# Kernel optimization log

Hardware: AMD Instinct MI355X
Metric: run time of the kernel (lower is better)

## Reference

```python
import jax, jax.numpy as jnp
import numpy as np

H, N, B, L = 256, 64, 4, 2048
LN_EPS = 1e-5


def setup_inputs() -> dict:
    key = jax.random.key(0)
    ks = jax.random.split(key, 10)
    u = jax.random.normal(ks[0], (B, L, H), dtype=jnp.float32)
    # Parameters (HiPPO-eig init replaced by equivalent-range random init; same forward math).
    log_neg_real = jnp.log(jax.random.uniform(ks[1], (N,), minval=0.01, maxval=2.0))
    imag = jax.random.normal(ks[2], (N,)) * 3.0
    B_re = jax.random.normal(ks[3], (H, N)) * 0.01
    B_im = jax.random.normal(ks[4], (H, N)) * 0.01
    C_re = jax.random.normal(ks[5], (H, N)) * 0.01
    C_im = jax.random.normal(ks[6], (H, N)) * 0.01
    D = jax.random.normal(ks[7], (H,)) * 0.01
    log_step = jax.random.uniform(ks[8], (H,), minval=-4.0, maxval=-1.0)
    ln_gamma = jnp.ones((H,), dtype=jnp.float32)
    ln_beta = jnp.zeros((H,), dtype=jnp.float32)
    return {"u": u, "log_neg_real": log_neg_real, "imag": imag,
            "B_re": B_re, "B_im": B_im, "C_re": C_re, "C_im": C_im,
            "D": D, "log_step": log_step, "ln_gamma": ln_gamma, "ln_beta": ln_beta}


def reference(u, log_neg_real, imag, B_re, B_im, C_re, C_im, D, log_step, ln_gamma, ln_beta):
    Bb, Ll, Hh = u.shape
    Lam_re = -jnp.exp(log_neg_real)                      # (N,)
    step = jnp.clip(jnp.exp(log_step), 1e-5, 1.0)        # (H,)
    s_re = step[:, None] * Lam_re[None, :]               # (H,N)
    s_im = step[:, None] * imag[None, :]                 # (H,N)
    Bb_re = B_re * step[:, None]
    Bb_im = B_im * step[:, None]
    CB_re = C_re * Bb_re - C_im * Bb_im                  # (H,N)
    CB_im = C_re * Bb_im + C_im * Bb_re                  # (H,N)
    l_idx = jnp.arange(Ll, dtype=u.dtype)                # (L,)
    ls_re = s_re[:, None, :] * l_idx[None, :, None]      # (H,L,N)
    ls_im = s_im[:, None, :] * l_idx[None, :, None]      # (H,L,N)
    mag = jnp.exp(ls_re)
    K = (jnp.einsum('hn,hln->hl', CB_re, mag * jnp.cos(ls_im))
         - jnp.einsum('hn,hln->hl', CB_im, mag * jnp.sin(ls_im)))  # (H,L)
    # FFT circular conv with zero padding to 2L -> linear conv
    uT = jnp.transpose(u, (0, 2, 1))                     # (B,H,L)
    n = 2 * Ll
    u_f = jnp.fft.rfft(uT, n=n)
    K_f = jnp.fft.rfft(K, n=n)
    y = jnp.fft.irfft(u_f * K_f[None], n=n)[..., :Ll]    # (B,H,L)
    y = y + uT * D[None, :, None]
    y = jnp.transpose(y, (0, 2, 1))                      # (B,L,H)
    y = jax.nn.gelu(y, approximate=False)                # torch nn.GELU default = exact
    # dropout: eval mode (identity)
    mean = jnp.mean(y, axis=-1, keepdims=True)
    var = jnp.var(y, axis=-1, keepdims=True)
    y = (y - mean) / jnp.sqrt(var + LN_EPS) * ln_gamma + ln_beta
    return y
```

## Files before the change

kernel.cpp:

```cpp
#include <hip/hip_runtime.h>
#include <hip/hip_bf16.h>
#include <math.h>

#define Hn 256
#define Nn 64
#define Bn 4
#define Ln 2048
#define Cn 64
#define NC 32

__global__ __launch_bounds__(256)
void k_pre(const float* __restrict__ u, float* __restrict__ uT,
           const float* __restrict__ lnr, const float* __restrict__ im,
           const float* __restrict__ Bre, const float* __restrict__ Bim,
           const float* __restrict__ Cre, const float* __restrict__ Cim,
           const float* __restrict__ lstep,
           float* __restrict__ G, float* __restrict__ apar,
           float* __restrict__ Krow)
{
    __shared__ float sh[64 * 65];
    int bid = blockIdx.x;
    int t   = threadIdx.x;

    if (bid < 512) {
        int b  = bid >> 7;
        int h0 = ((bid >> 5) & 3) << 6;
        int l0 = (bid & 31) << 6;
        int c4 = t & 15, rr = t >> 4;
        #pragma unroll
        for (int i = 0; i < 4; ++i) {
            int r = rr + (i << 4);
            float4 v = *(const float4*)&u[((size_t)b * Ln + l0 + r) * Hn + h0 + (c4 << 2)];
            sh[r * 65 + (c4 << 2) + 0] = v.x;
            sh[r * 65 + (c4 << 2) + 1] = v.y;
            sh[r * 65 + (c4 << 2) + 2] = v.z;
            sh[r * 65 + (c4 << 2) + 3] = v.w;
        }
        __syncthreads();
        #pragma unroll
        for (int i = 0; i < 4; ++i) {
            int hr = (t >> 4) + (i << 4);
            int lc = t & 15;
            float4 v;
            v.x = sh[((lc << 2) + 0) * 65 + hr];
            v.y = sh[((lc << 2) + 1) * 65 + hr];
            v.z = sh[((lc << 2) + 2) * 65 + hr];
            v.w = sh[((lc << 2) + 3) * 65 + hr];
            *(float4*)&uT[((size_t)b * Hn + h0 + hr) * Ln + l0 + (lc << 2)] = v;
        }
    } else {
        int h = bid - 512;
        int n = t;
        if (t < 64) {
            float st  = fminf(fmaxf(expf(lstep[h]), 1e-5f), 1.0f);
            float lam = -expf(lnr[n]);
            float er  = expf(st * lam);
            float sim = st * im[n];
            float ar  = er * cosf(sim);
            float ai  = er * sinf(sim);
            float bre = Bre[h * Nn + n] * st;
            float bim = Bim[h * Nn + n] * st;
            float cr  = Cre[h * Nn + n];
            float ci  = Cim[h * Nn + n];
            float CBr = cr * bre - ci * bim;
            float CBi = cr * bim + ci * bre;

            *(float2*)&apar[(h * Nn + n) * 2] = make_float2(ar, ai);

            float Pr = ar, Pi = ai;
            float Qr = 1.f, Qi = 0.f;
            for (int j = 0; j < 64; ++j) {
                *(float2*)&G[((h * 64 + j) * 64 + n) * 2] =
                    make_float2(CBr * Pr - CBi * Pi, CBr * Pi + CBi * Pr);
                sh[j * 65 + n] = CBr * Qr - CBi * Qi;
                float npr = Pr * ar - Pi * ai; Pi = Pr * ai + Pi * ar; Pr = npr;
                float nqr = Qr * ar - Qi * ai; Qi = Qr * ai + Qi * ar; Qr = nqr;
            }
        }
        __syncthreads();
        if (t < 64) {
            float s = 0.f;
            #pragma unroll
            for (int m = 0; m < 64; ++m) s += sh[t * 65 + m];
            Krow[h * 64 + t] = s;
        }
    }
}

__global__ __launch_bounds__(256, 4)
void k_scan_chunks(const float* __restrict__ uT, const float* __restrict__ apar,
                   const float* __restrict__ G, const float* __restrict__ Krow,
                   const float* __restrict__ D, float* __restrict__ ypre)
{
    int bh  = blockIdx.x;
    int h   = bh & (Hn - 1);
    int tid = threadIdx.x;
    int j   = tid & 63;
    int w   = __builtin_amdgcn_readfirstlane(tid >> 6);
    int n0  = w << 4;

    __shared__ float  kbuf[128];
    __shared__ float2 S_lds[NC][64];
    __shared__ float2 F_lds[4][64];
    __shared__ float  part[16][4][64];

    if (tid < 64) kbuf[tid] = 0.f;
    else if (tid < 128) kbuf[tid] = Krow[h * 64 + tid - 64];

    int n = j;
    float ar = apar[(h * Nn + n) * 2];
    float ai = apar[(h * Nn + n) * 2 + 1];
    float a2r = ar * ar - ai * ai;
    float a2i = 2.f * ar * ai;
    const float* uRow = uT + (size_t)bh * Ln;
    const float* useg = uRow + (w << 9);

    float2 Sloc[8];
    float xr = 0.f, xi = 0.f;
    #pragma unroll
    for (int k = 0; k < 8; ++k) {
        Sloc[k] = make_float2(xr, xi);
        const float4* up4 = (const float4*)(useg + (k << 6));
        #pragma unroll
        for (int q = 0; q < 16; ++q) {
            float4 uu = up4[q];
            float crr = fmaf(ar, uu.x, uu.y);
            float cii = ai * uu.x;
            float nxr = fmaf(a2r, xr, fmaf(-a2i, xi, crr));
            float nxi = fmaf(a2i, xr, fmaf(a2r, xi, cii));
            xr = nxr; xi = nxi;
            crr = fmaf(ar, uu.z, uu.w);
            cii = ai * uu.z;
            nxr = fmaf(a2r, xr, fmaf(-a2i, xi, crr));
            nxi = fmaf(a2i, xr, fmaf(a2r, xi, cii));
            xr = nxr; xi = nxi;
        }
    }
    F_lds[w][n] = make_float2(xr, xi);
    __syncthreads();

    float b_r = ar, b_i = ai;
    #pragma unroll
    for (int q = 0; q < 6; ++q) { float nr = b_r * b_r - b_i * b_i; b_i = 2.f * b_r * b_i; b_r = nr; }
    float p_r = b_r, p_i = b_i;
    #pragma unroll
    for (int q = 0; q < 3; ++q) { float nr = p_r * p_r - p_i * p_i; p_i = 2.f * p_r * p_i; p_r = nr; }

    float Xr = 0.f, Xi = 0.f;
    for (int s = 0; s < w; ++s) {
        float2 Ft = F_lds[s][n];
        float nXr = fmaf(p_r, Xr, fmaf(-p_i, Xi, Ft.x));
        float nXi = fmaf(p_i, Xr, fmaf(p_r, Xi, Ft.y));
        Xr = nXr; Xi = nXi;
    }

    float e_r = 1.f, e_i = 0.f;
    #pragma unroll
    for (int k = 0; k < 8; ++k) {
        float sr = Sloc[k].x + (e_r * Xr - e_i * Xi);
        float si = Sloc[k].y + (e_r * Xi + e_i * Xr);
        S_lds[(w << 3) + k][n] = make_float2(sr, si);
        float nr = e_r * b_r - e_i * b_i;
        e_i = e_r * b_i + e_i * b_r;
        e_r = nr;
    }
    __syncthreads();

    float4 Gr4[8];
    const float4* Gp4 = (const float4*)((const float2*)G + ((h * 64 + j) * 64 + n0));
    #pragma unroll
    for (int i = 0; i < 8; ++i) Gr4[i] = Gp4[i];
    float Kreg[16];
    #pragma unroll
    for (int i = 0; i < 16; ++i) Kreg[i] = kbuf[64 + j - n0 - i];

    float Dh = D[h];

    for (int half = 0; half < 2; ++half) {
        for (int cc = 0; cc < 16; ++cc) {
            int c = (half << 4) | cc;
            const float4* Sp4 = (const float4*)&S_lds[c][n0];
            const float4* uc4 = (const float4*)(uRow + (c << 6) + n0);
            float y0 = 0.f, y1 = 0.f, y2 = 0.f;
            #pragma unroll
            for (int i = 0; i < 8; ++i) {
                float4 sv = Sp4[i];
                y0 = fmaf(Gr4[i].x, sv.x, y0);
                y1 = fmaf(-Gr4[i].y, sv.y, y1);
                y0 = fmaf(Gr4[i].z, sv.z, y0);
                y1 = fmaf(-Gr4[i].w, sv.w, y1);
            }
            #pragma unroll
            for (int i = 0; i < 4; ++i) {
                float4 uu = uc4[i];
                y2 = fmaf(Kreg[4 * i + 0], uu.x, y2);
                y2 = fmaf(Kreg[4 * i + 1], uu.y, y2);
                y2 = fmaf(Kreg[4 * i + 2], uu.z, y2);
                y2 = fmaf(Kreg[4 * i + 3], uu.w, y2);
            }
            part[cc][w][j] = (y0 + y1) + y2;
        }
        __syncthreads();
        #pragma unroll
        for (int k = 0; k < 4; ++k) {
            int cc = (k << 2) | w;
            int c  = (half << 4) | cc;
            float y  = (part[cc][0][j] + part[cc][1][j]) + (part[cc][2][j] + part[cc][3][j]);
            float uv = uRow[(c << 6) + j];
            float yv = fmaf(Dh, uv, y);
            float g  = 0.5f * yv * (1.f + erff(yv * 0.70710678118654752f));
            ypre[(size_t)bh * Ln + (c << 6) + j] = g;
        }
        __syncthreads();
    }
}

__global__ __launch_bounds__(256)
void k_ln(const float* __restrict__ ypre, const float* __restrict__ gamma,
          const float* __restrict__ beta, float* __restrict__ out)
{
    __shared__ float tile[32][260];
    int b  = blockIdx.y;
    int l0 = blockIdx.x << 5;
    int t  = threadIdx.x;

    #pragma unroll
    for (int i = 0; i < 8; ++i) {
        int idx = (i << 8) + t;
        int hh  = idx >> 3, lo4 = idx & 7;
        float4 v = *(const float4*)&ypre[((size_t)b * Hn + hh) * Ln + l0 + (lo4 << 2)];
        tile[(lo4 << 2) + 0][hh] = v.x;
        tile[(lo4 << 2) + 1][hh] = v.y;
        tile[(lo4 << 2) + 2][hh] = v.z;
        tile[(lo4 << 2) + 3][hh] = v.w;
    }
    __syncthreads();

    int wv = t >> 6, lane = t & 63;
    float4 g4 = *(const float4*)&gamma[lane << 2];
    float4 b4 = *(const float4*)&beta[lane << 2];
    #pragma unroll
    for (int k = 0; k < 8; ++k) {
        int l = (k << 2) | wv;
        float4 v = *(const float4*)&tile[l][lane << 2];
        float sum = (v.x + v.y) + (v.z + v.w);
        float sq  = fmaf(v.x, v.x, fmaf(v.y, v.y, fmaf(v.z, v.z, v.w * v.w)));
        #pragma unroll
        for (int off = 32; off; off >>= 1) {
            sum += __shfl_xor(sum, off);
            sq  += __shfl_xor(sq, off);
        }
        float mean = sum * (1.f / 256.f);
        float var  = sq * (1.f / 256.f) - mean * mean;
        float rs   = rsqrtf(var + 1e-5f);
        float4 o;
        o.x = (v.x - mean) * rs * g4.x + b4.x;
        o.y = (v.y - mean) * rs * g4.y + b4.y;
        o.z = (v.z - mean) * rs * g4.z + b4.z;
        o.w = (v.w - mean) * rs * g4.w + b4.w;
        *(float4*)&out[((size_t)b * Ln + l0 + l) * Hn + (lane << 2)] = o;
    }
}

extern "C" void kernel_launch(void* const* d_in, const int* in_sizes, int n_in,
                              void* d_out, int out_size, void* d_ws, size_t ws_size,
                              hipStream_t stream)
{
    const float* u     = (const float*)d_in[0];
    const float* lnr   = (const float*)d_in[1];
    const float* im    = (const float*)d_in[2];
    const float* Bre   = (const float*)d_in[3];
    const float* Bim   = (const float*)d_in[4];
    const float* Cre   = (const float*)d_in[5];
    const float* Cim   = (const float*)d_in[6];
    const float* Dp    = (const float*)d_in[7];
    const float* lstep = (const float*)d_in[8];
    const float* gam   = (const float*)d_in[9];
    const float* bet   = (const float*)d_in[10];
    float* out = (float*)d_out;

    float* ws   = (float*)d_ws;
    float* uT   = ws;
    float* G    = uT   + (size_t)Bn * Hn * Ln;
    float* apar = G    + (size_t)Hn * 64 * Nn * 2;
    float* Krow = apar + (size_t)Hn * Nn * 2;
    float* ypre = Krow + (size_t)Hn * 64;

    k_pre<<<768, 256, 0, stream>>>(u, uT, lnr, im, Bre, Bim, Cre, Cim, lstep, G, apar, Krow);
    k_scan_chunks<<<Bn * Hn, 256, 0, stream>>>(uT, apar, G, Krow, Dp, ypre);
    k_ln<<<dim3(Ln / 32, Bn), 256, 0, stream>>>(ypre, gam, bet, out);
}
```

Before: 123.6 us.

## Recast chunked SSM scan as split-bf16 MFMA matmuls with precomputed fragments

```diff
diff --git a/kernel.cpp b/kernel.cpp
--- a/kernel.cpp
+++ b/kernel.cpp
@@ -6,8 +6,28 @@
 #define Nn 64
 #define Bn 4
 #define Ln 2048
-#define Cn 64
 #define NC 32
+
+typedef __attribute__((ext_vector_type(8))) short short8;
+typedef __attribute__((ext_vector_type(4))) float f32x4;
+
+#define MFMA16 __builtin_amdgcn_mfma_f32_16x16x32_bf16
+
+#define AF1_STRIDE 16384
+#define AF2_STRIDE 24576
+
+__device__ inline short bf16hi(float x) {
+    union { __hip_bfloat16 b; unsigned short u; } cv;
+    cv.b = __float2bfloat16(x);
+    return (short)cv.u;
+}
+__device__ inline float bf16f(short s) {
+    union { __hip_bfloat16 b; unsigned short u; } cv;
+    cv.u = (unsigned short)s;
+    return __bfloat162float(cv.b);
+}
+
+#define CSQ(r, i) { float _nr = (r)*(r) - (i)*(i); (i) = 2.f*(r)*(i); (r) = _nr; }
 
 __global__ __launch_bounds__(256)
 void k_pre(const float* __restrict__ u, float* __restrict__ uT,
@@ -15,203 +35,279 @@
            const float* __restrict__ Bre, const float* __restrict__ Bim,
            const float* __restrict__ Cre, const float* __restrict__ Cim,
            const float* __restrict__ lstep,
-           float* __restrict__ G, float* __restrict__ apar,
-           float* __restrict__ Krow)
+           short* __restrict__ AF1, short* __restrict__ AF2,
+           float* __restrict__ apar)
 {
-    __shared__ float sh[64 * 65];
+    __shared__ float sh[2][64][66];
+    __shared__ float cbrL[64];
+    __shared__ float kb[128];
     int bid = blockIdx.x;
-    int t   = threadIdx.x;
+    int tid = threadIdx.x;
 
     if (bid < 512) {
         int b  = bid >> 7;
         int h0 = ((bid >> 5) & 3) << 6;
         int l0 = (bid & 31) << 6;
-        int c4 = t & 15, rr = t >> 4;
+        int c4 = tid & 15, rr = tid >> 4;
         #pragma unroll
         for (int i = 0; i < 4; ++i) {
             int r = rr + (i << 4);
             float4 v = *(const float4*)&u[((size_t)b * Ln + l0 + r) * Hn + h0 + (c4 << 2)];
-            sh[r * 65 + (c4 << 2) + 0] = v.x;
-            sh[r * 65 + (c4 << 2) + 1] = v.y;
-            sh[r * 65 + (c4 << 2) + 2] = v.z;
-            sh[r * 65 + (c4 << 2) + 3] = v.w;
+            sh[0][r][(c4 << 2) + 0] = v.x;
+            sh[0][r][(c4 << 2) + 1] = v.y;
+            sh[0][r][(c4 << 2) + 2] = v.z;
+            sh[0][r][(c4 << 2) + 3] = v.w;
         }
         __syncthreads();
         #pragma unroll
         for (int i = 0; i < 4; ++i) {
-            int hr = (t >> 4) + (i << 4);
-            int lc = t & 15;
+            int hr = (tid >> 4) + (i << 4);
+            int lc = tid & 15;
             float4 v;
-            v.x = sh[((lc << 2) + 0) * 65 + hr];
-            v.y = sh[((lc << 2) + 1) * 65 + hr];
-            v.z = sh[((lc << 2) + 2) * 65 + hr];
-            v.w = sh[((lc << 2) + 3) * 65 + hr];
+            v.x = sh[0][(lc << 2) + 0][hr];
+            v.y = sh[0][(lc << 2) + 1][hr];
+            v.z = sh[0][(lc << 2) + 2][hr];
+            v.w = sh[0][(lc << 2) + 3][hr];
             *(float4*)&uT[((size_t)b * Hn + h0 + hr) * Ln + l0 + (lc << 2)] = v;
         }
-    } else {
-        int h = bid - 512;
-        int n = t;
-        if (t < 64) {
-            float st  = fminf(fmaxf(expf(lstep[h]), 1e-5f), 1.0f);
-            float lam = -expf(lnr[n]);
-            float er  = expf(st * lam);
-            float sim = st * im[n];
-            float ar  = er * cosf(sim);
-            float ai  = er * sinf(sim);
-            float bre = Bre[h * Nn + n] * st;
-            float bim = Bim[h * Nn + n] * st;
-            float cr  = Cre[h * Nn + n];
-            float ci  = Cim[h * Nn + n];
-            float CBr = cr * bre - ci * bim;
-            float CBi = cr * bim + ci * bre;
-
-            *(float2*)&apar[(h * Nn + n) * 2] = make_float2(ar, ai);
-
-            float Pr = ar, Pi = ai;
-            float Qr = 1.f, Qi = 0.f;
-            for (int j = 0; j < 64; ++j) {
-                *(float2*)&G[((h * 64 + j) * 64 + n) * 2] =
-                    make_float2(CBr * Pr - CBi * Pi, CBr * Pi + CBi * Pr);
-                sh[j * 65 + n] = CBr * Qr - CBi * Qi;
-                float npr = Pr * ar - Pi * ai; Pi = Pr * ai + Pi * ar; Pr = npr;
-                float nqr = Qr * ar - Qi * ai; Qi = Qr * ai + Qi * ar; Qr = nqr;
-            }
-        }
-        __syncthreads();
-        if (t < 64) {
-            float s = 0.f;
+        return;
+    }
+
+    int h    = bid - 512;
+    int lane = tid & 63;
+    int wv   = tid >> 6;
+    int kq   = lane >> 4;
+    int l15  = lane & 15;
+    int mrow = (wv << 4) + l15;
+
+    float st  = fminf(fmaxf(expf(lstep[h]), 1e-5f), 1.0f);
+    float lam = -expf(lnr[lane]);
+    float er  = expf(st * lam);
+    float smv = st * im[lane];
+    float ar  = er * cosf(smv);
+    float ai  = er * sinf(smv);
+    float bre = Bre[h * Nn + lane] * st;
+    float bim = Bim[h * Nn + lane] * st;
+    float crr = Cre[h * Nn + lane];
+    float cii = Cim[h * Nn + lane];
+    float cbr = crr * bre - cii * bim;
+    float cbi = crr * bim + cii * bre;
+
+    float a16r = ar, a16i = ai;
+    CSQ(a16r, a16i); CSQ(a16r, a16i); CSQ(a16r, a16i); CSQ(a16r, a16i);
+    float a32r = a16r, a32i = a16i; CSQ(a32r, a32i);
+    float a48r = a32r * a16r - a32i * a16i;
+    float a48i = a32r * a16i + a32i * a16r;
+    float a64r = a32r, a64i = a32i; CSQ(a64r, a64i);
+    if (tid < 64) {
+        apar[(h * Nn + lane) * 2]     = a64r;
+        apar[(h * Nn + lane) * 2 + 1] = a64i;
+    }
+
+    float pr = 1.f, pi = 0.f;
+    if (wv == 1) { pr = a16r; pi = a16i; }
+    else if (wv == 2) { pr = a32r; pi = a32i; }
+    else if (wv == 3) { pr = a48r; pi = a48i; }
+    for (int i = 0; i < 16; ++i) {
+        int t = 63 - ((wv << 4) + i);
+        sh[0][lane][t] = pr;
+        sh[1][lane][t] = pi;
+        float nr = pr * ar - pi * ai; pi = pr * ai + pi * ar; pr = nr;
+    }
+    __syncthreads();
+
+    short* A1h = AF1 + (size_t)h * AF1_STRIDE;
+    #pragma unroll
+    for (int cm = 0; cm < 2; ++cm)
+        #pragma unroll
+        for (int kt = 0; kt < 2; ++kt) {
+            union { short s[8]; short8 v; } uh, ul;
             #pragma unroll
-            for (int m = 0; m < 64; ++m) s += sh[t * 65 + m];
-            Krow[h * 64 + t] = s;
-        }
+            for (int j = 0; j < 8; ++j) {
+                float x = sh[cm][mrow][kt * 32 + kq * 8 + j];
+                short hh = bf16hi(x);
+                uh.s[j] = hh;
+                ul.s[j] = bf16hi(x - bf16f(hh));
+            }
+            *(short8*)&A1h[(((cm * 2 + 0) * 4 + wv) * 2 + kt) * 512 + lane * 8] = uh.v;
+            *(short8*)&A1h[(((cm * 2 + 1) * 4 + wv) * 2 + kt) * 512 + lane * 8] = ul.v;
+        }
+    __syncthreads();
+
+    if (tid < 64) {
+        cbrL[lane] = cbr;
+        float Pr = ar, Pi = ai;
+        for (int j = 0; j < 64; ++j) {
+            sh[0][j][lane] = cbr * Pr - cbi * Pi;
+            sh[1][j][lane] = cbr * Pi + cbi * Pr;
+            float nr = Pr * ar - Pi * ai; Pi = Pr * ai + Pi * ar; Pr = nr;
+        }
+    }
+    __syncthreads();
+    if (tid < 64) kb[tid] = 0.f;
+    else if (tid < 128) {
+        int t2 = tid - 64;
+        float s = 0.f;
+        if (t2 == 0) { for (int n2 = 0; n2 < 64; ++n2) s += cbrL[n2]; }
+        else         { for (int n2 = 0; n2 < 64; ++n2) s += sh[0][t2 - 1][n2]; }
+        kb[tid] = s;
+    }
+    __syncthreads();
+
+    short* A2h = AF2 + (size_t)h * AF2_STRIDE;
+    #pragma unroll
+    for (int kt = 0; kt < 6; ++kt) {
+        union { short s[8]; short8 v; } uh, ul;
+        #pragma unroll
+        for (int j = 0; j < 8; ++j) {
+            float x;
+            if (kt < 2) {
+                int kk = kt * 32 + kq * 8 + j;
+                x = kb[64 + mrow - kk];
+            } else {
+                int q2 = kt - 2;
+                int nn = (q2 & 1) * 32 + kq * 8 + j;
+                x = (q2 >> 1) ? -sh[1][mrow][nn] : sh[0][mrow][nn];
+            }
+            short hh = bf16hi(x);
+            uh.s[j] = hh;
+            ul.s[j] = bf16hi(x - bf16f(hh));
+        }
+        *(short8*)&A2h[((0 * 4 + wv) * 6 + kt) * 512 + lane * 8] = uh.v;
+        *(short8*)&A2h[((1 * 4 + wv) * 6 + kt) * 512 + lane * 8] = ul.v;
     }
 }
 
 __global__ __launch_bounds__(256, 4)
 void k_scan_chunks(const float* __restrict__ uT, const float* __restrict__ apar,
-                   const float* __restrict__ G, const float* __restrict__ Krow,
+                   const short* __restrict__ AF1, const short* __restrict__ AF2,
                    const float* __restrict__ D, float* __restrict__ ypre)
 {
-    int bh  = blockIdx.x;
-    int h   = bh & (Hn - 1);
-    int tid = threadIdx.x;
-    int j   = tid & 63;
-    int w   = __builtin_amdgcn_readfirstlane(tid >> 6);
-    int n0  = w << 4;
-
-    __shared__ float  kbuf[128];
-    __shared__ float2 S_lds[NC][64];
-    __shared__ float2 F_lds[4][64];
-    __shared__ float  part[16][4][64];
-
-    if (tid < 64) kbuf[tid] = 0.f;
-    else if (tid < 128) kbuf[tid] = Krow[h * 64 + tid - 64];
-
-    int n = j;
-    float ar = apar[(h * Nn + n) * 2];
-    float ai = apar[(h * Nn + n) * 2 + 1];
-    float a2r = ar * ar - ai * ai;
-    float a2i = 2.f * ar * ai;
+    __shared__ float P2[64][35][2];
+    __shared__ short Sb[2][2][32][72];
+
+    int bh   = blockIdx.x;
+    int h    = bh & (Hn - 1);
+    int tid  = threadIdx.x;
+    int lane = tid & 63;
+    int w    = __builtin_amdgcn_readfirstlane(tid >> 6);
+    int l15  = lane & 15;
+    int kq   = lane >> 4;
+
     const float* uRow = uT + (size_t)bh * Ln;
-    const float* useg = uRow + (w << 9);
-
-    float2 Sloc[8];
-    float xr = 0.f, xi = 0.f;
-    #pragma unroll
-    for (int k = 0; k < 8; ++k) {
-        Sloc[k] = make_float2(xr, xi);
-        const float4* up4 = (const float4*)(useg + (k << 6));
-        #pragma unroll
-        for (int q = 0; q < 16; ++q) {
-            float4 uu = up4[q];
-            float crr = fmaf(ar, uu.x, uu.y);
-            float cii = ai * uu.x;
-            float nxr = fmaf(a2r, xr, fmaf(-a2i, xi, crr));
-            float nxi = fmaf(a2i, xr, fmaf(a2r, xi, cii));
-            xr = nxr; xi = nxi;
-            crr = fmaf(ar, uu.z, uu.w);
-            cii = ai * uu.z;
-            nxr = fmaf(a2r, xr, fmaf(-a2i, xi, crr));
-            nxi = fmaf(a2i, xr, fmaf(a2r, xi, cii));
-            xr = nxr; xi = nxi;
-        }
-    }
-    F_lds[w][n] = make_float2(xr, xi);
-    __syncthreads();
-
-    float b_r = ar, b_i = ai;
-    #pragma unroll
-    for (int q = 0; q < 6; ++q) { float nr = b_r * b_r - b_i * b_i; b_i = 2.f * b_r * b_i; b_r = nr; }
-    float p_r = b_r, p_i = b_i;
-    #pragma unroll
-    for (int q = 0; q < 3; ++q) { float nr = p_r * p_r - p_i * p_i; p_i = 2.f * p_r * p_i; p_r = nr; }
-
-    float Xr = 0.f, Xi = 0.f;
-    for (int s = 0; s < w; ++s) {
-        float2 Ft = F_lds[s][n];
-        float nXr = fmaf(p_r, Xr, fmaf(-p_i, Xi, Ft.x));
-        float nXi = fmaf(p_i, Xr, fmaf(p_r, Xi, Ft.y));
-        Xr = nXr; Xi = nXi;
-    }
-
-    float e_r = 1.f, e_i = 0.f;
-    #pragma unroll
-    for (int k = 0; k < 8; ++k) {
-        float sr = Sloc[k].x + (e_r * Xr - e_i * Xi);
-        float si = Sloc[k].y + (e_r * Xi + e_i * Xr);
-        S_lds[(w << 3) + k][n] = make_float2(sr, si);
-        float nr = e_r * b_r - e_i * b_i;
-        e_i = e_r * b_i + e_i * b_r;
-        e_r = nr;
-    }
-    __syncthreads();
-
-    float4 Gr4[8];
-    const float4* Gp4 = (const float4*)((const float2*)G + ((h * 64 + j) * 64 + n0));
-    #pragma unroll
-    for (int i = 0; i < 8; ++i) Gr4[i] = Gp4[i];
-    float Kreg[16];
-    #pragma unroll
-    for (int i = 0; i < 16; ++i) Kreg[i] = kbuf[64 + j - n0 - i];
+    const short* A1h  = AF1 + (size_t)h * AF1_STRIDE;
+    const short* A2h  = AF2 + (size_t)h * AF2_STRIDE;
+
+    short8 Uh[2][2], Ul[2][2];
+    #pragma unroll
+    for (int kt = 0; kt < 2; ++kt)
+        #pragma unroll
+        for (int ct = 0; ct < 2; ++ct) {
+            int c = ct * 16 + l15;
+            const float* up = uRow + c * 64 + kt * 32 + kq * 8;
+            float4 f0 = *(const float4*)up;
+            float4 f1 = *(const float4*)(up + 4);
+            float xv[8] = {f0.x, f0.y, f0.z, f0.w, f1.x, f1.y, f1.z, f1.w};
+            union { short s[8]; short8 v; } hh, ll;
+            #pragma unroll
+            for (int j = 0; j < 8; ++j) {
+                short hs = bf16hi(xv[j]);
+                hh.s[j] = hs;
+                ll.s[j] = bf16hi(xv[j] - bf16f(hs));
+            }
+            Uh[kt][ct] = hh.v;
+            Ul[kt][ct] = ll.v;
+        }
+
+    f32x4 Pre_acc[2] = {{0.f,0.f,0.f,0.f},{0.f,0.f,0.f,0.f}};
+    f32x4 Pim_acc[2] = {{0.f,0.f,0.f,0.f},{0.f,0.f,0.f,0.f}};
+    #pragma unroll
+    for (int kt = 0; kt < 2; ++kt) {
+        short8 a_re_h = *(const short8*)&A1h[((0 * 4 + w) * 2 + kt) * 512 + lane * 8];
+        short8 a_re_l = *(const short8*)&A1h[((1 * 4 + w) * 2 + kt) * 512 + lane * 8];
+        short8 a_im_h = *(const short8*)&A1h[((2 * 4 + w) * 2 + kt) * 512 + lane * 8];
+        short8 a_im_l = *(const short8*)&A1h[((3 * 4 + w) * 2 + kt) * 512 + lane * 8];
+        #pragma unroll
+        for (int ct = 0; ct < 2; ++ct) {
+            Pre_acc[ct] = MFMA16(a_re_h, Uh[kt][ct], Pre_acc[ct], 0, 0, 0);
+            Pre_acc[ct] = MFMA16(a_re_h, Ul[kt][ct], Pre_acc[ct], 0, 0, 0);
+            Pre_acc[ct] = MFMA16(a_re_l, Uh[kt][ct], Pre_acc[ct], 0, 0, 0);
+            Pim_acc[ct] = MFMA16(a_im_h, Uh[kt][ct], Pim_acc[ct], 0, 0, 0);
+            Pim_acc[ct] = MFMA16(a_im_h, Ul[kt][ct], Pim_acc[ct], 0, 0, 0);
+            Pim_acc[ct] = MFMA16(a_im_l, Uh[kt][ct], Pim_acc[ct], 0, 0, 0);
+        }
+    }
+    #pragma unroll
+    for (int ct = 0; ct < 2; ++ct)
+        #pragma unroll
+        for (int r = 0; r < 4; ++r) {
+            int n = (w << 4) + kq * 4 + r;
+            int c = ct * 16 + l15;
+            *(float2*)&P2[n][c][0] = make_float2(Pre_acc[ct][r], Pim_acc[ct][r]);
+        }
+    __syncthreads();
+
+    {
+        int n = lane;
+        float a64r = apar[(h * Nn + n) * 2];
+        float a64i = apar[(h * Nn + n) * 2 + 1];
+        float sr = 0.f, si = 0.f;
+        for (int c = 0; c < NC; ++c) {
+            if ((c >> 3) == w) {
+                short hr = bf16hi(sr); short lr = bf16hi(sr - bf16f(hr));
+                short hi2 = bf16hi(si); short li = bf16hi(si - bf16f(hi2));
+                Sb[0][0][c][n] = hr;  Sb[1][0][c][n] = lr;
+                Sb[0][1][c][n] = hi2; Sb[1][1][c][n] = li;
+            }
+            float2 pv = *(float2*)&P2[n][c][0];
+            float nsr = fmaf(a64r, sr, fmaf(-a64i, si, pv.x));
+            float nsi = fmaf(a64i, sr, fmaf(a64r, si, pv.y));
+            sr = nsr; si = nsi;
+        }
+    }
+    __syncthreads();
+
+    f32x4 Yacc[2] = {{0.f,0.f,0.f,0.f},{0.f,0.f,0.f,0.f}};
+    #pragma unroll
+    for (int kt = 0; kt < 6; ++kt) {
+        short8 a_h = *(const short8*)&A2h[((0 * 4 + w) * 6 + kt) * 512 + lane * 8];
+        short8 a_l = *(const short8*)&A2h[((1 * 4 + w) * 6 + kt) * 512 + lane * 8];
+        #pragma unroll
+        for (int ct = 0; ct < 2; ++ct) {
+            short8 bhf, blf;
+            if (kt < 2) { bhf = Uh[kt][ct]; blf = Ul[kt][ct]; }
+            else {
+                int q2 = kt - 2, reim = q2 >> 1;
+                int nb = (q2 & 1) * 32 + kq * 8;
+                int c  = ct * 16 + l15;
+                bhf = *(const short8*)&Sb[0][reim][c][nb];
+                blf = *(const short8*)&Sb[1][reim][c][nb];
+            }
+            Yacc[ct] = MFMA16(a_h, bhf, Yacc[ct], 0, 0, 0);
+            Yacc[ct] = MFMA16(a_h, blf, Yacc[ct], 0, 0, 0);
+            Yacc[ct] = MFMA16(a_l, bhf, Yacc[ct], 0, 0, 0);
+        }
+    }
+    float* Yl = (float*)P2;
+    #pragma unroll
+    for (int ct = 0; ct < 2; ++ct)
+        #pragma unroll
+        for (int r = 0; r < 4; ++r) {
+            int j = (w << 4) + kq * 4 + r;
+            int c = ct * 16 + l15;
+            Yl[j * 70 + c] = Yacc[ct][r];
+        }
+    __syncthreads();
 
     float Dh = D[h];
-
-    for (int half = 0; half < 2; ++half) {
-        for (int cc = 0; cc < 16; ++cc) {
-            int c = (half << 4) | cc;
-            const float4* Sp4 = (const float4*)&S_lds[c][n0];
-            const float4* uc4 = (const float4*)(uRow + (c << 6) + n0);
-            float y0 = 0.f, y1 = 0.f, y2 = 0.f;
-            #pragma unroll
-            for (int i = 0; i < 8; ++i) {
-                float4 sv = Sp4[i];
-                y0 = fmaf(Gr4[i].x, sv.x, y0);
-                y1 = fmaf(-Gr4[i].y, sv.y, y1);
-                y0 = fmaf(Gr4[i].z, sv.z, y0);
-                y1 = fmaf(-Gr4[i].w, sv.w, y1);
-            }
-            #pragma unroll
-            for (int i = 0; i < 4; ++i) {
-                float4 uu = uc4[i];
-                y2 = fmaf(Kreg[4 * i + 0], uu.x, y2);
-                y2 = fmaf(Kreg[4 * i + 1], uu.y, y2);
-                y2 = fmaf(Kreg[4 * i + 2], uu.z, y2);
-                y2 = fmaf(Kreg[4 * i + 3], uu.w, y2);
-            }
-            part[cc][w][j] = (y0 + y1) + y2;
-        }
-        __syncthreads();
-        #pragma unroll
-        for (int k = 0; k < 4; ++k) {
-            int cc = (k << 2) | w;
-            int c  = (half << 4) | cc;
-            float y  = (part[cc][0][j] + part[cc][1][j]) + (part[cc][2][j] + part[cc][3][j]);
-            float uv = uRow[(c << 6) + j];
-            float yv = fmaf(Dh, uv, y);
-            float g  = 0.5f * yv * (1.f + erff(yv * 0.70710678118654752f));
-            ypre[(size_t)bh * Ln + (c << 6) + j] = g;
-        }
-        __syncthreads();
+    #pragma unroll
+    for (int i = 0; i < 8; ++i) {
+        int c = (w << 3) + i;
+        float y  = Yl[lane * 70 + c];
+        float uv = uRow[c * 64 + lane];
+        float yv = fmaf(Dh, uv, y);
+        float g  = 0.5f * yv * (1.f + erff(yv * 0.70710678118654752f));
+        ypre[(size_t)bh * Ln + c * 64 + lane] = g;
     }
 }
 
@@ -281,12 +377,12 @@
 
     float* ws   = (float*)d_ws;
     float* uT   = ws;
-    float* G    = uT   + (size_t)Bn * Hn * Ln;
-    float* apar = G    + (size_t)Hn * 64 * Nn * 2;
-    float* Krow = apar + (size_t)Hn * Nn * 2;
-    float* ypre = Krow + (size_t)Hn * 64;
-
-    k_pre<<<768, 256, 0, stream>>>(u, uT, lnr, im, Bre, Bim, Cre, Cim, lstep, G, apar, Krow);
-    k_scan_chunks<<<Bn * Hn, 256, 0, stream>>>(uT, apar, G, Krow, Dp, ypre);
+    float* apar = uT + (size_t)Bn * Hn * Ln;
+    float* ypre = apar + (size_t)Hn * Nn * 2;
+    short* AF1  = (short*)(ypre + (size_t)Bn * Hn * Ln);
+    short* AF2  = AF1 + (size_t)Hn * AF1_STRIDE;
+
+    k_pre<<<768, 256, 0, stream>>>(u, uT, lnr, im, Bre, Bim, Cre, Cim, lstep, AF1, AF2, apar);
+    k_scan_chunks<<<Bn * Hn, 256, 0, stream>>>(uT, apar, AF1, AF2, Dp, ypre);
     k_ln<<<dim3(Ln / 32, Bn), 256, 0, stream>>>(ypre, gam, bet, out);
 }
```

Measured after the change: 106.4 us. 13.9% less time.
